# Kernel optimization log

Measured on AMD Instinct MI355X. Metric: run time of the kernel, lower is better.

## Reference

```python
import jax, jax.numpy as jnp
import numpy as np

N = 262144          # number of coordinate points
IN = 3              # coordinate dim
FF = 256            # fourier feature dim (out_features)
NFREQ = FF // 2     # 128 frequencies
H = 256             # mlp hidden width
L = 4               # hidden sine layers
OUT = 2             # Fullmodel hard-codes out_features=2 for the MLP
OMEGA0 = 30.0


def setup_inputs() -> dict:
    key = jax.random.key(0)
    ks = jax.random.split(key, 12)
    x = jax.random.normal(ks[0], (N, IN), dtype=jnp.float32)
    # Fourier encoder params (non-trainable in torch, still float inputs here)
    scales = jnp.ones((1, IN), dtype=jnp.float32)  # coordinate_scales = [1,1,1]
    B = jax.random.normal(ks[1], (IN, NFREQ), dtype=jnp.float32) * 3.0 * 10.0  # N(0,3)*10
    # SIREN first layer: uniform(-1/in, 1/in), in = FF
    W0 = jax.random.uniform(ks[2], (H, FF), dtype=jnp.float32, minval=-1.0 / FF, maxval=1.0 / FF)
    b0 = jax.random.uniform(ks[3], (H,), dtype=jnp.float32, minval=-1.0 / np.sqrt(FF), maxval=1.0 / np.sqrt(FF))
    # Hidden sine layers: uniform(-sqrt(6/in), sqrt(6/in)), in = H
    c = float(np.sqrt(6.0 / H))
    Wh = jax.random.uniform(ks[4], (L, H, H), dtype=jnp.float32, minval=-c, maxval=c)
    bh = jax.random.uniform(ks[5], (L, H), dtype=jnp.float32, minval=-1.0 / np.sqrt(H), maxval=1.0 / np.sqrt(H))
    # Final plain linear H -> OUT (default torch init, any small values fine)
    Wf = jax.random.uniform(ks[6], (OUT, H), dtype=jnp.float32, minval=-1.0 / np.sqrt(H), maxval=1.0 / np.sqrt(H))
    bf = jax.random.uniform(ks[7], (OUT,), dtype=jnp.float32, minval=-1.0 / np.sqrt(H), maxval=1.0 / np.sqrt(H))
    return {"x": x, "scales": scales, "B": B, "W0": W0, "b0": b0,
            "Wh": Wh, "bh": bh, "Wf": Wf, "bf": bf}


def reference(x, scales, B, W0, b0, Wh, bh, Wf, bf):
    # Fourier feature map: sqrt(2) * [sin(proj), cos(proj)]
    proj = (x * scales) @ B                                   # [N, NFREQ]
    sqrt2 = jnp.float32(np.sqrt(2.0))
    h = jnp.concatenate([jnp.sin(proj), jnp.cos(proj)], axis=-1) * sqrt2  # [N, FF]
    # First SIREN layer: sin(omega0 * (W x + b))
    h = jnp.sin(OMEGA0 * (h @ W0.T + b0))                     # [N, H]
    # Hidden sine layers: sin(W x + b)
    for i in range(L):
        h = jnp.sin(h @ Wh[i].T + bh[i])                      # [N, H]
    return h @ Wf.T + bf                                      # [N, OUT]
```

## Files before the change

### kernel.cpp

```cpp
#include <hip/hip_runtime.h>
#include <hip/hip_bf16.h>


typedef __attribute__((ext_vector_type(8))) short bf16x8;
typedef __attribute__((ext_vector_type(4))) float f32x4;

#define NTOTAL 262144
#define BM 64
#define HD 256
#define INV2PI 0.15915494309189535f

__device__ __forceinline__ unsigned short f2bf(float f) {
    unsigned int u = __float_as_uint(f);
    u += 0x7FFFu + ((u >> 16) & 1u);
    return (unsigned short)(u >> 16);
}

__device__ __forceinline__ unsigned int pk2(float a, float b) {
    __hip_bfloat162 h = __float22bfloat162_rn(make_float2(a, b));
    union { __hip_bfloat162 h; unsigned int u; } c;
    c.h = h;
    return c.u;
}

__device__ __forceinline__ int a_off(int r, int byte) {
    return r * 512 + (byte ^ ((r & 15) << 4));
}

__global__ void convert_w(const float* __restrict__ W0, const float* __restrict__ Wh,
                          const float* __restrict__ Wf, const float* __restrict__ b0,
                          const float* __restrict__ bh, unsigned short* __restrict__ wb) {
    const int i = blockIdx.x * 256 + threadIdx.x;
    if (i < 327680) {
        const int l = i >> 16, rem = i & 65535;
        const int j = rem >> 8, k = rem & 255;
        const float sc = (l == 0) ? (1.41421356237309515f * 30.0f * INV2PI) : INV2PI;
        const float v = ((l == 0) ? W0[rem] : Wh[i - 65536]) * sc;
        const int jt = j >> 4, kt = k >> 5, q = (k >> 3) & 3, r = j & 15, t = k & 7;
        const int dst = (l << 16) + (((jt << 3) + kt) << 9) + (((q << 4) + r) << 3) + t;
        wb[dst] = f2bf(v);
    }
    if (i < 4096)
        wb[327680 + i] = (i < 512) ? f2bf(Wf[i]) : (unsigned short)0;
    if (i < 1280) {
        const int l = i >> 8, j = i & 255;
        const float sc = (l == 0) ? (30.0f * INV2PI) : INV2PI;
        float* bsc = (float*)(wb + 331776);
        bsc[i] = ((l == 0) ? b0[j] : bh[i - 256]) * sc;
    }
}

__global__ __launch_bounds__(256, 3) void siren_fused(
    const float* __restrict__ x, const float* __restrict__ scales,
    const float* __restrict__ Bm, const float* __restrict__ bfin,
    const unsigned short* __restrict__ wb, float* __restrict__ out) {

    __shared__ __align__(16) unsigned short A[BM * HD];

    const int tid  = threadIdx.x;
    const int lane = tid & 63;
    const int wid  = tid >> 6;
    const int row0 = blockIdx.x * BM;
    const int arow = lane & 15;
    const int q    = lane >> 4;
    const int kq   = q * 8;
    const float* bsc = (const float*)(wb + 331776);

    bf16x8 wfbuf[2][4];
    #pragma unroll
    for (int jt = 0; jt < 4; ++jt)
        wfbuf[0][jt] = *(const bf16x8*)(wb + (((wid * 4 + jt) << 3) << 9) + lane * 8);

    {
        const int r  = tid >> 2;
        const int c0 = (tid & 3) * 32;
        const float* xr = x + (row0 + r) * 3;
        const float x0 = xr[0] * scales[0] * INV2PI;
        const float x1 = xr[1] * scales[1] * INV2PI;
        const float x2 = xr[2] * scales[2] * INV2PI;
        #pragma unroll
        for (int cc = 0; cc < 32; cc += 8) {
            const int c = c0 + cc;
            float sv[8], cv[8];
            #pragma unroll
            for (int t = 0; t < 8; ++t) {
                const float rev = x0 * Bm[c + t] + x1 * Bm[128 + c + t] + x2 * Bm[256 + c + t];
                sv[t] = __builtin_amdgcn_sinf(rev);
                cv[t] = __builtin_amdgcn_cosf(rev);
            }
            uint4 us, uc;
            us.x = pk2(sv[0], sv[1]); us.y = pk2(sv[2], sv[3]);
            us.z = pk2(sv[4], sv[5]); us.w = pk2(sv[6], sv[7]);
            uc.x = pk2(cv[0], cv[1]); uc.y = pk2(cv[2], cv[3]);
            uc.z = pk2(cv[4], cv[5]); uc.w = pk2(cv[6], cv[7]);
            *(uint4*)((char*)A + a_off(r, 2 * c))         = us;
            *(uint4*)((char*)A + a_off(r, 2 * (c + 128))) = uc;
        }
    }

    #pragma unroll 1
    for (int layer = 0; layer < 5; ++layer) {
        const unsigned short* Wl = wb + (layer << 16);
        const float* bl = bsc + layer * HD;

        __syncthreads();

        f32x4 acc[4][4];
        #pragma unroll
        for (int jt = 0; jt < 4; ++jt) {
            const float4 bv = *(const float4*)(bl + wid * 64 + jt * 16 + q * 4);
            #pragma unroll
            for (int rt = 0; rt < 4; ++rt) {
                acc[jt][rt][0] = bv.x; acc[jt][rt][1] = bv.y;
                acc[jt][rt][2] = bv.z; acc[jt][rt][3] = bv.w;
            }
        }

        #pragma unroll
        for (int kt = 0; kt < 8; ++kt) {
            const int cur = kt & 1, nxt = cur ^ 1;
            bf16x8 hf[4];
            #pragma unroll
            for (int rt = 0; rt < 4; ++rt)
                hf[rt] = *(const bf16x8*)((const char*)A +
                    a_off(rt * 16 + arow, kt * 64 + q * 16));
            if (kt < 7) {
                #pragma unroll
                for (int jt = 0; jt < 4; ++jt)
                    wfbuf[nxt][jt] = *(const bf16x8*)(Wl +
                        ((((wid * 4 + jt) << 3) + kt + 1) << 9) + lane * 8);
            }
            #pragma unroll
            for (int jt = 0; jt < 4; ++jt)
                #pragma unroll
                for (int rt = 0; rt < 4; ++rt)
                    acc[jt][rt] = __builtin_amdgcn_mfma_f32_16x16x32_bf16(
                        wfbuf[cur][jt], hf[rt], acc[jt][rt], 0, 0, 0);
        }

        if (layer < 4) {
            const unsigned short* Wn = wb + ((layer + 1) << 16);
            #pragma unroll
            for (int jt = 0; jt < 4; ++jt)
                wfbuf[0][jt] = *(const bf16x8*)(Wn + (((wid * 4 + jt) << 3) << 9) + lane * 8);
        }

        __syncthreads();

        #pragma unroll
        for (int jt = 0; jt < 4; ++jt) {
            const int jj = wid * 64 + jt * 16 + q * 4;
            #pragma unroll
            for (int rt = 0; rt < 4; ++rt) {
                const int r = rt * 16 + arow;
                const float s0 = __builtin_amdgcn_sinf(acc[jt][rt][0]);
                const float s1 = __builtin_amdgcn_sinf(acc[jt][rt][1]);
                const float s2 = __builtin_amdgcn_sinf(acc[jt][rt][2]);
                const float s3 = __builtin_amdgcn_sinf(acc[jt][rt][3]);
                uint2 val;
                val.x = pk2(s0, s1);
                val.y = pk2(s2, s3);
                *(uint2*)((char*)A + a_off(r, jj * 2)) = val;
            }
        }
    }

    __syncthreads();

    {
        const unsigned short* Wfp = wb + 327680;
        f32x4 acc = (f32x4)(0.0f);
        #pragma unroll
        for (int kt = 0; kt < 8; ++kt) {
            const bf16x8 ff = *(const bf16x8*)(Wfp + arow * HD + kt * 32 + kq);
            const bf16x8 hf = *(const bf16x8*)((const char*)A +
                a_off(wid * 16 + arow, kt * 64 + q * 16));
            acc = __builtin_amdgcn_mfma_f32_16x16x32_bf16(ff, hf, acc, 0, 0, 0);
        }
        if (q == 0) {
            const int rg = row0 + wid * 16 + arow;
            float2 o;
            o.x = acc[0] + bfin[0];
            o.y = acc[1] + bfin[1];
            *(float2*)(out + rg * 2) = o;
        }
    }
}

extern "C" void kernel_launch(void* const* d_in, const int* in_sizes, int n_in,
                              void* d_out, int out_size, void* d_ws, size_t ws_size,
                              hipStream_t stream) {
    (void)in_sizes; (void)n_in; (void)out_size; (void)ws_size;
    const float* x      = (const float*)d_in[0];
    const float* scales = (const float*)d_in[1];
    const float* Bm     = (const float*)d_in[2];
    const float* W0     = (const float*)d_in[3];
    const float* b0     = (const float*)d_in[4];
    const float* Wh     = (const float*)d_in[5];
    const float* bh     = (const float*)d_in[6];
    const float* Wf     = (const float*)d_in[7];
    const float* bf     = (const float*)d_in[8];
    unsigned short* wb  = (unsigned short*)d_ws;

    hipLaunchKernelGGL(convert_w, dim3(1280), dim3(256), 0, stream,
                       W0, Wh, Wf, b0, bh, wb);
    hipLaunchKernelGGL(siren_fused, dim3(NTOTAL / BM), dim3(256), 0, stream,
                       x, scales, Bm, bf, wb, (float*)d_out);
}
```

Baseline: 191.7 us.

## Switch hidden-layer GEMMs from 16x16x32 to 32x32x16 MFMA tiles

```diff
diff --git a/kernel.cpp b/kernel.cpp
--- a/kernel.cpp
+++ b/kernel.cpp
@@ -4,6 +4,7 @@
 
 typedef __attribute__((ext_vector_type(8))) short bf16x8;
 typedef __attribute__((ext_vector_type(4))) float f32x4;
+typedef __attribute__((ext_vector_type(16))) float f32x16;
 
 #define NTOTAL 262144
 #define BM 64
@@ -36,8 +37,9 @@
         const int j = rem >> 8, k = rem & 255;
         const float sc = (l == 0) ? (1.41421356237309515f * 30.0f * INV2PI) : INV2PI;
         const float v = ((l == 0) ? W0[rem] : Wh[i - 65536]) * sc;
-        const int jt = j >> 4, kt = k >> 5, q = (k >> 3) & 3, r = j & 15, t = k & 7;
-        const int dst = (l << 16) + (((jt << 3) + kt) << 9) + (((q << 4) + r) << 3) + t;
+        const int jg = j >> 5, jr = j & 31;
+        const int ks = k >> 4, hi = (k >> 3) & 1, t = k & 7;
+        const int dst = (l << 16) + (((jg << 4) + ks) << 9) + (((hi << 5) + jr) << 3) + t;
         wb[dst] = f2bf(v);
     }
     if (i < 4096)
@@ -61,15 +63,16 @@
     const int lane = tid & 63;
     const int wid  = tid >> 6;
     const int row0 = blockIdx.x * BM;
+    const int ln31 = lane & 31;
+    const int hi   = lane >> 5;
     const int arow = lane & 15;
     const int q    = lane >> 4;
-    const int kq   = q * 8;
     const float* bsc = (const float*)(wb + 331776);
 
-    bf16x8 wfbuf[2][4];
+    bf16x8 wabuf[2][2];
     #pragma unroll
-    for (int jt = 0; jt < 4; ++jt)
-        wfbuf[0][jt] = *(const bf16x8*)(wb + (((wid * 4 + jt) << 3) << 9) + lane * 8);
+    for (int jt2 = 0; jt2 < 2; ++jt2)
+        wabuf[0][jt2] = *(const bf16x8*)(wb + (((wid * 2 + jt2) << 4) << 9) + lane * 8);
 
     {
         const int r  = tid >> 2;
@@ -105,62 +108,70 @@
 
         __syncthreads();
 
-        f32x4 acc[4][4];
-        #pragma unroll
-        for (int jt = 0; jt < 4; ++jt) {
-            const float4 bv = *(const float4*)(bl + wid * 64 + jt * 16 + q * 4);
-            #pragma unroll
-            for (int rt = 0; rt < 4; ++rt) {
-                acc[jt][rt][0] = bv.x; acc[jt][rt][1] = bv.y;
-                acc[jt][rt][2] = bv.z; acc[jt][rt][3] = bv.w;
-            }
-        }
-
-        #pragma unroll
-        for (int kt = 0; kt < 8; ++kt) {
-            const int cur = kt & 1, nxt = cur ^ 1;
-            bf16x8 hf[4];
-            #pragma unroll
-            for (int rt = 0; rt < 4; ++rt)
-                hf[rt] = *(const bf16x8*)((const char*)A +
-                    a_off(rt * 16 + arow, kt * 64 + q * 16));
-            if (kt < 7) {
-                #pragma unroll
-                for (int jt = 0; jt < 4; ++jt)
-                    wfbuf[nxt][jt] = *(const bf16x8*)(Wl +
-                        ((((wid * 4 + jt) << 3) + kt + 1) << 9) + lane * 8);
-            }
-            #pragma unroll
-            for (int jt = 0; jt < 4; ++jt)
-                #pragma unroll
-                for (int rt = 0; rt < 4; ++rt)
-                    acc[jt][rt] = __builtin_amdgcn_mfma_f32_16x16x32_bf16(
-                        wfbuf[cur][jt], hf[rt], acc[jt][rt], 0, 0, 0);
+        f32x16 acc[2][2];
+        #pragma unroll
+        for (int jt2 = 0; jt2 < 2; ++jt2) {
+            #pragma unroll
+            for (int g2 = 0; g2 < 4; ++g2) {
+                const float4 bv = *(const float4*)(bl + wid * 64 + jt2 * 32 + g2 * 8 + hi * 4);
+                #pragma unroll
+                for (int rt2 = 0; rt2 < 2; ++rt2) {
+                    acc[jt2][rt2][g2 * 4 + 0] = bv.x;
+                    acc[jt2][rt2][g2 * 4 + 1] = bv.y;
+                    acc[jt2][rt2][g2 * 4 + 2] = bv.z;
+                    acc[jt2][rt2][g2 * 4 + 3] = bv.w;
+                }
+            }
+        }
+
+        #pragma unroll
+        for (int ks = 0; ks < 16; ++ks) {
+            const int cur = ks & 1, nxt = cur ^ 1;
+            bf16x8 hb[2];
+            #pragma unroll
+            for (int rt2 = 0; rt2 < 2; ++rt2)
+                hb[rt2] = *(const bf16x8*)((const char*)A +
+                    a_off(rt2 * 32 + ln31, ks * 32 + hi * 16));
+            if (ks < 15) {
+                #pragma unroll
+                for (int jt2 = 0; jt2 < 2; ++jt2)
+                    wabuf[nxt][jt2] = *(const bf16x8*)(Wl +
+                        ((((wid * 2 + jt2) << 4) + ks + 1) << 9) + lane * 8);
+            }
+            #pragma unroll
+            for (int jt2 = 0; jt2 < 2; ++jt2)
+                #pragma unroll
+                for (int rt2 = 0; rt2 < 2; ++rt2)
+                    acc[jt2][rt2] = __builtin_amdgcn_mfma_f32_32x32x16_bf16(
+                        wabuf[cur][jt2], hb[rt2], acc[jt2][rt2], 0, 0, 0);
         }
 
         if (layer < 4) {
             const unsigned short* Wn = wb + ((layer + 1) << 16);
             #pragma unroll
-            for (int jt = 0; jt < 4; ++jt)
-                wfbuf[0][jt] = *(const bf16x8*)(Wn + (((wid * 4 + jt) << 3) << 9) + lane * 8);
+            for (int jt2 = 0; jt2 < 2; ++jt2)
+                wabuf[0][jt2] = *(const bf16x8*)(Wn + (((wid * 2 + jt2) << 4) << 9) + lane * 8);
         }
 
         __syncthreads();
 
         #pragma unroll
-        for (int jt = 0; jt < 4; ++jt) {
-            const int jj = wid * 64 + jt * 16 + q * 4;
-            #pragma unroll
-            for (int rt = 0; rt < 4; ++rt) {
-                const int r = rt * 16 + arow;
-                const float s0 = __builtin_amdgcn_sinf(acc[jt][rt][0]);
-                const float s1 = __builtin_amdgcn_sinf(acc[jt][rt][1]);
-                const float s2 = __builtin_amdgcn_sinf(acc[jt][rt][2]);
-                const float s3 = __builtin_amdgcn_sinf(acc[jt][rt][3]);
-                uint2 val;
-                val.x = pk2(s0, s1);
-                val.y = pk2(s2, s3);
-                *(uint2*)((char*)A + a_off(r, jj * 2)) = val;
+        for (int jt2 = 0; jt2 < 2; ++jt2) {
+            #pragma unroll
+            for (int rt2 = 0; rt2 < 2; ++rt2) {
+                const int r = rt2 * 32 + ln31;
+                #pragma unroll
+                for (int g2 = 0; g2 < 4; ++g2) {
+                    const int j0 = wid * 64 + jt2 * 32 + g2 * 8 + hi * 4;
+                    const float s0 = __builtin_amdgcn_sinf(acc[jt2][rt2][g2 * 4 + 0]);
+                    const float s1 = __builtin_amdgcn_sinf(acc[jt2][rt2][g2 * 4 + 1]);
+                    const float s2 = __builtin_amdgcn_sinf(acc[jt2][rt2][g2 * 4 + 2]);
+                    const float s3 = __builtin_amdgcn_sinf(acc[jt2][rt2][g2 * 4 + 3]);
+                    uint2 val;
+                    val.x = pk2(s0, s1);
+                    val.y = pk2(s2, s3);
+                    *(uint2*)((char*)A + a_off(r, j0 * 2)) = val;
+                }
             }
         }
     }
@@ -172,7 +183,7 @@
         f32x4 acc = (f32x4)(0.0f);
         #pragma unroll
         for (int kt = 0; kt < 8; ++kt) {
-            const bf16x8 ff = *(const bf16x8*)(Wfp + arow * HD + kt * 32 + kq);
+            const bf16x8 ff = *(const bf16x8*)(Wfp + arow * HD + kt * 32 + q * 8);
             const bf16x8 hf = *(const bf16x8*)((const char*)A +
                 a_off(wid * 16 + arow, kt * 64 + q * 16));
             acc = __builtin_amdgcn_mfma_f32_16x16x32_bf16(ff, hf, acc, 0, 0, 0);
```

Result: slower. 225.8 us (+17.8%).
